# Performance work log

Measured on AMD Instinct MI355X. Metric: run time of the kernel, lower is better.

## Reference

```python
import jax, jax.numpy as jnp
import numpy as np

H, D, LORA = 12, 64, 64  # n_heads, headdim, decay-LoRA rank


def _time_mix(x, mu, w_bias, dw1, dw2, u, Wr, Wk, Wv, Wg, Wo, ln_w, ln_b):
    """RWKV-6 time-mix (single direction). x: (B,T,C)."""
    B, T, C = x.shape
    # token shift: previous token (zero-padded at t=0)
    xs = jnp.concatenate([jnp.zeros_like(x[:, :1]), x[:, :-1]], axis=1)
    dx = xs - x
    xr, xk, xv, xw, xg = (x + dx * mu[i] for i in range(5))  # order: r,k,v,w,g
    r = (xr @ Wr).reshape(B, T, H, D)
    k = (xk @ Wk).reshape(B, T, H, D)
    v = (xv @ Wv).reshape(B, T, H, D)
    g = jax.nn.silu(xg @ Wg)                                   # (B,T,C)
    # data-dependent per-channel decay in (0,1)
    w = jnp.exp(-jnp.exp(w_bias + jnp.tanh(xw @ dw1) @ dw2)).reshape(B, T, H, D)

    def step(S, rkvw):  # S: (B,H,D,D) state
        r_t, k_t, v_t, w_t = rkvw          # each (B,H,D)
        kv = k_t[..., None] * v_t[:, :, None, :]               # (B,H,D,D)
        y_t = jnp.einsum('bhd,bhde->bhe', r_t, S + u[None, :, :, None] * kv)
        return w_t[..., None] * S + kv, y_t

    seq = tuple(jnp.moveaxis(a, 1, 0) for a in (r, k, v, w))   # (T,B,H,D)
    S0 = jnp.zeros((B, H, D, D), x.dtype)
    _, ys = jax.lax.scan(step, S0, seq)
    y = jnp.moveaxis(ys, 0, 1)                                 # (B,T,H,D)
    # per-head GroupNorm (n_heads groups over d_model)
    mean = y.mean(-1, keepdims=True)
    var = y.var(-1, keepdims=True)
    y = ((y - mean) * jax.lax.rsqrt(var + 1e-5)).reshape(B, T, C) * ln_w + ln_b
    return (y * g) @ Wo


def reference(x, pad_mask, mu, w_bias, dw1, dw2, u, Wr, Wk, Wv, Wg, Wo, ln_w, ln_b):
    p = lambda i: (mu[i], w_bias[i], dw1[i], dw2[i], u[i], Wr[i], Wk[i], Wv[i],
                   Wg[i], Wo[i], ln_w[i], ln_b[i])
    fwd_out = _time_mix(x, *p(0))
    bwd_out = _time_mix(x[:, ::-1], *p(1))[:, ::-1]
    out = fwd_out + bwd_out
    out = out * pad_mask[..., None].astype(out.dtype)
    return out


def setup_inputs() -> dict:
    key = jax.random.key(0)
    ks = jax.random.split(key, 12)
    B, T, C = 4, 1024, 768
    s = C ** -0.5
    return {
        'x': jax.random.normal(ks[0], (B, T, C), jnp.float32),
        'pad_mask': jnp.ones((B, T), jnp.bool_),
        'mu': jax.random.uniform(ks[1], (2, 5, C), jnp.float32),
        'w_bias': jax.random.normal(ks[2], (2, C), jnp.float32) * 0.3 - 0.5,
        'dw1': jax.random.normal(ks[3], (2, C, LORA), jnp.float32) * s,
        'dw2': jax.random.normal(ks[4], (2, LORA, C), jnp.float32) * 0.1,
        'u': jax.random.normal(ks[5], (2, H, D), jnp.float32) * 0.5,
        'Wr': jax.random.normal(ks[6], (2, C, C), jnp.float32) * s,
        'Wk': jax.random.normal(ks[7], (2, C, C), jnp.float32) * s,
        'Wv': jax.random.normal(ks[8], (2, C, C), jnp.float32) * s,
        'Wg': jax.random.normal(ks[9], (2, C, C), jnp.float32) * s,
        'Wo': jax.random.normal(ks[10], (2, C, C), jnp.float32) * s,
        'ln_w': jnp.ones((2, C), jnp.float32),
        'ln_b': jnp.zeros((2, C), jnp.float32),
    }
```

## Files before the change

kernel.cpp:

```cpp
#include <hip/hip_runtime.h>
#include <cstdint>
#include <cstddef>


#define HH   12
#define DD   64
#define CC   768
#define TT   1024
#define BBB  4
#define LR   64
#define BT   (BBB*TT)
#define WSQ  (CC*CC)

typedef unsigned short u16;
typedef _Float16 f16x8 __attribute__((ext_vector_type(8)));
typedef float f32x4 __attribute__((ext_vector_type(4)));

__device__ __forceinline__ u16 f2h(float f) {
    const _Float16 h = (_Float16)f;
    return __builtin_bit_cast(u16, h);
}
__device__ __forceinline__ float h2f(u16 h) {
    return (float)__builtin_bit_cast(_Float16, h);
}

__device__ __forceinline__ void gl_lds16(const void* g, void* l) {
    __builtin_amdgcn_global_load_lds(
        (const __attribute__((address_space(1))) void*)g,
        (__attribute__((address_space(3))) void*)l, 16, 0, 0);
}

__device__ __forceinline__ float mask_val(const void* mp, int idx) {
    const unsigned char* b = (const unsigned char*)mp;
    const int i0 = ((const int*)mp)[0];
    if (i0 == 0x3f800000) {
        return ((const float*)mp)[idx] != 0.f ? 1.f : 0.f;
    }
    if ((b[1] | b[2] | b[3]) == 0) {
        return ((const int*)mp)[idx] != 0 ? 1.f : 0.f;
    }
    return b[idx] ? 1.f : 0.f;
}

struct TP10 { const float* src[10]; };

__global__ __launch_bounds__(256)
void transpose_conv(TP10 tj, u16* __restrict__ dst)
{
    __shared__ float sh[32][33];
    const int j = blockIdx.z;
    const float* __restrict__ src = tj.src[j];
    u16* __restrict__ d = dst + (size_t)j * WSQ;
    const int n0 = blockIdx.x << 5, k0 = blockIdx.y << 5;
    const int tx = threadIdx.x & 31, ty = threadIdx.x >> 5;
    #pragma unroll
    for (int i = 0; i < 4; ++i)
        sh[ty + (i << 3)][tx] = src[(size_t)(k0 + ty + (i << 3)) * CC + n0 + tx];
    __syncthreads();
    #pragma unroll
    for (int i = 0; i < 4; ++i)
        d[(size_t)(n0 + ty + (i << 3)) * CC + k0 + tx] =
            f2h(sh[tx][ty + (i << 3)]);
}

__global__ __launch_bounds__(256)
void convert_x(const float* __restrict__ x, u16* __restrict__ xb)
{
    const size_t off = ((size_t)blockIdx.x * 256 + threadIdx.x) * 8;
    const float4 a = *reinterpret_cast<const float4*>(x + off);
    const float4 b = *reinterpret_cast<const float4*>(x + off + 4);
    uint4 w;
    w.x = (unsigned)f2h(a.x) | ((unsigned)f2h(a.y) << 16);
    w.y = (unsigned)f2h(a.z) | ((unsigned)f2h(a.w) << 16);
    w.z = (unsigned)f2h(b.x) | ((unsigned)f2h(b.y) << 16);
    w.w = (unsigned)f2h(b.z) | ((unsigned)f2h(b.w) << 16);
    *reinterpret_cast<uint4*>(xb + off) = w;
}

__global__ __launch_bounds__(256)
void convert_mu(const float* __restrict__ mu, u16* __restrict__ muh, int n)
{
    const int i = blockIdx.x * 256 + threadIdx.x;
    if (i < n) muh[i] = f2h(mu[i]);
}

__global__ __launch_bounds__(256)
void mix4_kernel(const u16* __restrict__ xb, const u16* __restrict__ muh,
                 u16* __restrict__ mx, const int dbase)
{
    const int j = blockIdx.y;
    const int slot = blockIdx.z;
    const int dir = dbase + slot;
    const int idx = blockIdx.x * 256 + threadIdx.x;
    const int s = idx / 96;
    const int c = (idx - s * 96) << 3;
    const int b = s >> 10, ts = s & (TT - 1);
    const int t = dir ? (TT - 1 - ts) : ts;
    const int tp = dir ? (t + 1) : (t - 1);
    const int musel = (j == 3) ? 4 : j;

    const uint4 xa4 = *reinterpret_cast<const uint4*>(
        xb + (size_t)(b * TT + t) * CC + c);
    uint4 xp4 = make_uint4(0u, 0u, 0u, 0u);
    if (ts > 0)
        xp4 = *reinterpret_cast<const uint4*>(
            xb + (size_t)(b * TT + tp) * CC + c);
    const uint4 m4 = *reinterpret_cast<const uint4*>(
        muh + (size_t)dir * 5 * CC + musel * CC + c);

    const f16x8 xa = __builtin_bit_cast(f16x8, xa4);
    const f16x8 xp = __builtin_bit_cast(f16x8, xp4);
    const f16x8 mm = __builtin_bit_cast(f16x8, m4);
    const f16x8 res = (xp - xa) * mm + xa;

    u16* __restrict__ dst = mx + (size_t)((slot << 2) + j) * ((size_t)BT * CC);
    *reinterpret_cast<uint4*>(dst + (size_t)s * CC + c) =
        __builtin_bit_cast(uint4, res);
}

struct GB { const u16* Wt[8]; const u16* Ab[8]; float* out[8];
            const float* mu[8]; int act[8]; int dirv[8]; };

__global__ __launch_bounds__(256)
void gemm_mfma_big(GB p, const u16* __restrict__ xb,
                   const int K, const int N, const int mixA)
{
    const int j = blockIdx.z;
    const u16* __restrict__ Wt = p.Wt[j];
    const u16* __restrict__ Ab = p.Ab[j];
    float* __restrict__ out = p.out[j];
    const float* __restrict__ mu = p.mu[j];
    const int act = p.act[j];
    const int dir = p.dirv[j];

    __shared__ __align__(16) u16 Als[128][64];
    __shared__ __align__(16) u16 Bls[128][64];
    const int tid = threadIdx.x;
    const int rowbase = blockIdx.x << 7;
    const int colbase = blockIdx.y << 7;
    const int lane = tid & 63;
    const int wid = tid >> 6;
    const int wr = (wid >> 1) << 6;
    const int wc = (wid & 1) << 6;
    const int lm = lane & 15;

    const int lrow = lane >> 3;
    const int gcol = (((lane & 7) ^ lrow) << 3);

    f32x4 acc[4][4] = {};

    for (int k0 = 0; k0 < K; k0 += 64) {
        if (mixA) {
            #pragma unroll
            for (int it = 0; it < 4; ++it) {
                const int c   = tid + (it << 8);
                const int row = c >> 3;
                const int ch  = c & 7;
                const int kq  = (ch ^ (row & 7)) << 3;
                *reinterpret_cast<uint4*>(&Bls[row][ch << 3]) =
                    *reinterpret_cast<const uint4*>(
                        Wt + (size_t)(colbase + row) * K + k0 + kq);
                const int s  = rowbase + row;
                const int bb = s >> 10, ts = s & (TT - 1);
                const int t  = dir ? (TT - 1 - ts) : ts;
                const int tp = dir ? (t + 1) : (t - 1);
                const uint4 xa4 = *reinterpret_cast<const uint4*>(
                    xb + (size_t)(bb * TT + t) * CC + k0 + kq);
                uint4 xp4 = make_uint4(0u, 0u, 0u, 0u);
                if (ts > 0)
                    xp4 = *reinterpret_cast<const uint4*>(
                        xb + (size_t)(bb * TT + tp) * CC + k0 + kq);
                const u16* as = reinterpret_cast<const u16*>(&xa4);
                const u16* ps = reinterpret_cast<const u16*>(&xp4);
                const float4 m0 = *reinterpret_cast<const float4*>(mu + k0 + kq);
                const float4 m1 = *reinterpret_cast<const float4*>(mu + k0 + kq + 4);
                const float mm[8] = {m0.x, m0.y, m0.z, m0.w,
                                     m1.x, m1.y, m1.z, m1.w};
                uint4 w;
                unsigned rr[4];
                #pragma unroll
                for (int q = 0; q < 4; ++q) {
                    const float a0 = h2f(as[2 * q]);
                    const float a1 = h2f(as[2 * q + 1]);
                    const float p0 = h2f(ps[2 * q]);
                    const float p1 = h2f(ps[2 * q + 1]);
                    const float v0 = fmaf(p0 - a0, mm[2 * q], a0);
                    const float v1 = fmaf(p1 - a1, mm[2 * q + 1], a1);
                    rr[q] = (unsigned)f2h(v0) | ((unsigned)f2h(v1) << 16);
                }
                w.x = rr[0]; w.y = rr[1]; w.z = rr[2]; w.w = rr[3];
                *reinterpret_cast<uint4*>(&Als[row][ch << 3]) = w;
            }
        } else {
            #pragma unroll
            for (int i = 0; i < 4; ++i) {
                const int rb  = (wid << 5) + (i << 3);
                const int row = rb + lrow;
                gl_lds16(Ab + (size_t)(rowbase + row) * K + k0 + gcol,
                         &Als[rb][0]);
                gl_lds16(Wt + (size_t)(colbase + row) * K + k0 + gcol,
                         &Bls[rb][0]);
            }
        }
        __syncthreads();
        #pragma unroll
        for (int ks = 0; ks < 2; ++ks) {
            const int gc = (ks << 2) + (lane >> 4);
            const int sl = (gc ^ (lm & 7)) << 3;
            f16x8 av[4], bv[4];
            #pragma unroll
            for (int mi = 0; mi < 4; ++mi)
                av[mi] = *reinterpret_cast<const f16x8*>(
                    &Als[wr + mi * 16 + lm][sl]);
            #pragma unroll
            for (int ni = 0; ni < 4; ++ni)
                bv[ni] = *reinterpret_cast<const f16x8*>(
                    &Bls[wc + ni * 16 + lm][sl]);
            #pragma unroll
            for (int mi = 0; mi < 4; ++mi)
                #pragma unroll
                for (int ni = 0; ni < 4; ++ni)
                    acc[mi][ni] = __builtin_amdgcn_mfma_f32_16x16x32_f16(
                        av[mi], bv[ni], acc[mi][ni], 0, 0, 0);
        }
        __syncthreads();
    }

    #pragma unroll
    for (int mi = 0; mi < 4; ++mi) {
        #pragma unroll
        for (int r = 0; r < 4; ++r) {
            const int srow = rowbase + wr + mi * 16 + ((lane >> 4) << 2) + r;
            if (act <= 1) {
                #pragma unroll
                for (int ni = 0; ni < 4; ++ni) {
                    float v = acc[mi][ni][r];
                    if (act == 1) v = v / (1.f + expf(-v));
                    out[(size_t)srow * N + colbase + wc + ni * 16 + lm] = v;
                }
            } else {
                const int b2  = srow >> 10;
                const int ts2 = srow & (TT - 1);
                const int t2  = dir ? (TT - 1 - ts2) : ts2;
                float* op = out + (size_t)(b2 * TT + t2) * CC + colbase + wc + lm;
                #pragma unroll
                for (int ni = 0; ni < 4; ++ni)
                    op[ni * 16] = acc[mi][ni][r];
            }
        }
    }
}

__global__ __launch_bounds__(256)
void combine_kernel(float* __restrict__ out, const float* __restrict__ obuf,
                    const void* __restrict__ mask)
{
    const size_t idx = ((size_t)blockIdx.x * 256 + threadIdx.x) * 4;
    const int row = (int)(idx / CC);
    const float mv = mask_val(mask, row);
    const float4 a = *reinterpret_cast<const float4*>(out + idx);
    const float4 b = *reinterpret_cast<const float4*>(obuf + idx);
    *reinterpret_cast<float4*>(out + idx) = make_float4(
        (a.x + b.x) * mv, (a.y + b.y) * mv, (a.z + b.z) * mv, (a.w + b.w) * mv);
}

__global__ __launch_bounds__(256)
void lora1_kernel(const float* __restrict__ x, const float* __restrict__ mu,
                  const float* __restrict__ dw1, float* __restrict__ out,
                  const int dbase)
{
    __shared__ float As[16][68];
    __shared__ float Bs[64][68];
    const int tid = threadIdx.x;
    const int rowbase = blockIdx.x << 4;
    const int slot = blockIdx.y;
    const int dir = dbase + slot;
    const float* __restrict__ muD = mu + (size_t)dir * 5 * CC + 3 * CC;
    const float* __restrict__ dw1p = dw1 + (size_t)dir * CC * LR;
    float* __restrict__ outp = out + (size_t)slot * BT * LR;

    const int arow = tid >> 4;
    const int akq  = (tid & 15) << 2;
    const int s  = rowbase + arow;
    const int bb = s >> 10, ts = s & (TT - 1);
    const int t  = dir ? (TT - 1 - ts) : ts;
    const int tp = dir ? (t + 1) : (t - 1);

    const int c0 = tid & 63;
    const int r4 = tid >> 6;

    float acc[4] = {0.f, 0.f, 0.f, 0.f};

    for (int k0 = 0; k0 < CC; k0 += 64) {
        {
            const int c = k0 + akq;
            const float4 xa = *reinterpret_cast<const float4*>(
                x + (size_t)(bb * TT + t) * CC + c);
            float4 xp = make_float4(0.f, 0.f, 0.f, 0.f);
            if (ts > 0)
                xp = *reinterpret_cast<const float4*>(
                    x + (size_t)(bb * TT + tp) * CC + c);
            const float4 m4 = *reinterpret_cast<const float4*>(muD + c);
            float4 va;
            va.x = fmaf(xp.x - xa.x, m4.x, xa.x);
            va.y = fmaf(xp.y - xa.y, m4.y, xa.y);
            va.z = fmaf(xp.z - xa.z, m4.z, xa.z);
            va.w = fmaf(xp.w - xa.w, m4.w, xa.w);
            *reinterpret_cast<float4*>(&As[arow][akq]) = va;
        }
        #pragma unroll
        for (int it = 0; it < 4; ++it) {
            const int c2 = tid + (it << 8);
            const int brow = c2 >> 4, bcol = (c2 & 15) << 2;
            *reinterpret_cast<float4*>(&Bs[brow][bcol]) =
                *reinterpret_cast<const float4*>(
                    dw1p + (size_t)(k0 + brow) * LR + bcol);
        }
        __syncthreads();
        #pragma unroll
        for (int k4 = 0; k4 < 16; ++k4) {
            float bv[4];
            #pragma unroll
            for (int q = 0; q < 4; ++q) bv[q] = Bs[(k4 << 2) + q][c0];
            #pragma unroll
            for (int i = 0; i < 4; ++i) {
                const float4 a4 = *reinterpret_cast<const float4*>(
                    &As[r4 + (i << 2)][k4 << 2]);
                acc[i] = fmaf(a4.x, bv[0], acc[i]);
                acc[i] = fmaf(a4.y, bv[1], acc[i]);
                acc[i] = fmaf(a4.z, bv[2], acc[i]);
                acc[i] = fmaf(a4.w, bv[3], acc[i]);
            }
        }
        __syncthreads();
    }
    #pragma unroll
    for (int i = 0; i < 4; ++i)
        outp[(size_t)(rowbase + r4 + (i << 2)) * LR + c0] = tanhf(acc[i]);
}

__global__ __launch_bounds__(256)
void gemm_kernel(const float* __restrict__ lora, const float* __restrict__ dw2,
                 const float* __restrict__ wbias, float* __restrict__ wwbuf,
                 const int dbase)
{
    __shared__ float As[16][68];
    __shared__ float Bs[16][68];
    const int tid = threadIdx.x;
    const int rowbase = blockIdx.x << 6;
    const int colbase = blockIdx.y << 6;
    const int slot = blockIdx.z;
    const int dir = dbase + slot;
    const float* __restrict__ Ap = lora + (size_t)slot * BT * LR;
    const float* __restrict__ W  = dw2 + (size_t)dir * LR * CC;
    const float* __restrict__ bias = wbias + (size_t)dir * CC;
    float* __restrict__ out = wwbuf + (size_t)slot * BT * CC;

    const int ty = tid >> 4, tx = tid & 15;
    const int am = tid >> 2;
    const int aq = tid & 3;
    const int s  = rowbase + am;
    const int bk = tid >> 4;
    const int bn = (tid & 15) << 2;

    float acc[4][4];
    #pragma unroll
    for (int i = 0; i < 4; ++i)
        #pragma unroll
        for (int j = 0; j < 4; ++j) acc[i][j] = 0.f;

    for (int k0 = 0; k0 < LR; k0 += 16) {
        const float4 va = *reinterpret_cast<const float4*>(
            Ap + (size_t)s * LR + k0 + (aq << 2));
        const float4 vb = *reinterpret_cast<const float4*>(
            W + (size_t)(k0 + bk) * CC + colbase + bn);
        As[(aq << 2) + 0][am] = va.x;
        As[(aq << 2) + 1][am] = va.y;
        As[(aq << 2) + 2][am] = va.z;
        As[(aq << 2) + 3][am] = va.w;
        *reinterpret_cast<float4*>(&Bs[bk][bn]) = vb;
        __syncthreads();
        #pragma unroll
        for (int kk = 0; kk < 16; ++kk) {
            const float4 a  = *reinterpret_cast<const float4*>(&As[kk][ty << 2]);
            const float4 bv = *reinterpret_cast<const float4*>(&Bs[kk][tx << 2]);
            const float av[4]  = {a.x, a.y, a.z, a.w};
            const float bvv[4] = {bv.x, bv.y, bv.z, bv.w};
            #pragma unroll
            for (int i = 0; i < 4; ++i)
                #pragma unroll
                for (int j = 0; j < 4; ++j)
                    acc[i][j] = fmaf(av[i], bvv[j], acc[i][j]);
        }
        __syncthreads();
    }

    #pragma unroll
    for (int i = 0; i < 4; ++i) {
        const int srow = rowbase + (ty << 2) + i;
        const int ncol = colbase + (tx << 2);
        float v[4];
        #pragma unroll
        for (int j = 0; j < 4; ++j)
            v[j] = expf(-expf(acc[i][j] + bias[ncol + j]));
        *reinterpret_cast<float4*>(out + (size_t)srow * CC + ncol) =
            make_float4(v[0], v[1], v[2], v[3]);
    }
}

template<int L>
__global__ __launch_bounds__(64)
void scanA_kernel(const float* __restrict__ kbuf, const float* __restrict__ vbuf,
                  const float* __restrict__ wbuf,
                  float* __restrict__ SL, float* __restrict__ Pbuf)
{
    constexpr int NCHL = TT / L;
    constexpr size_t SLN = (size_t)NCHL * BBB * HH * DD * DD;
    constexpr size_t PN  = (size_t)NCHL * BBB * HH * DD;
    __shared__ float lk[L * DD], lw[L * DD], lv[L * DD];
    const int c = blockIdx.x, h = blockIdx.y;
    const int b = blockIdx.z & (BBB - 1);
    const int slot = blockIdx.z >> 2;
    const size_t boff = (size_t)slot * BT * CC;
    const int e = threadIdx.x;
    const int rowq = e >> 4;
    const int col  = (e & 15) << 2;

    const size_t gbase = boff + (size_t)(b * TT + c * L) * CC + h * DD;
    #pragma unroll
    for (int r4 = 0; r4 < L / 4; ++r4) {
        const int row = (r4 << 2) + rowq;
        const size_t ga = gbase + (size_t)row * CC + col;
        *reinterpret_cast<float4*>(&lk[row * DD + col]) =
            *reinterpret_cast<const float4*>(kbuf + ga);
        *reinterpret_cast<float4*>(&lw[row * DD + col]) =
            *reinterpret_cast<const float4*>(wbuf + ga);
        *reinterpret_cast<float4*>(&lv[row * DD + col]) =
            *reinterpret_cast<const float4*>(vbuf + ga);
    }
    __syncthreads();

    float S[DD];
    #pragma unroll
    for (int d = 0; d < DD; ++d) S[d] = 0.f;
    float P = 1.f;

    for (int t = 0; t < L; ++t) {
        const float ve = lv[t * DD + e];
        P *= lw[t * DD + e];
        #pragma unroll
        for (int d4 = 0; d4 < 16; ++d4) {
            const float4 k4 = *reinterpret_cast<const float4*>(&lk[t * DD + (d4 << 2)]);
            const float4 w4 = *reinterpret_cast<const float4*>(&lw[t * DD + (d4 << 2)]);
            S[(d4 << 2) + 0] = fmaf(w4.x, S[(d4 << 2) + 0], k4.x * ve);
            S[(d4 << 2) + 1] = fmaf(w4.y, S[(d4 << 2) + 1], k4.y * ve);
            S[(d4 << 2) + 2] = fmaf(w4.z, S[(d4 << 2) + 2], k4.z * ve);
            S[(d4 << 2) + 3] = fmaf(w4.w, S[(d4 << 2) + 3], k4.w * ve);
        }
    }

    float* slotp = SL + (size_t)slot * SLN
                 + (size_t)((c * BBB + b) * HH + h) * DD * DD;
    #pragma unroll
    for (int d = 0; d < DD; ++d) slotp[d * DD + e] = S[d];
    Pbuf[(size_t)slot * PN + (size_t)((c * BBB + b) * HH + h) * DD + e] = P;
}

__global__ __launch_bounds__(64)
void scanB_kernel(float* __restrict__ SL, const float* __restrict__ Pbuf,
                  const int nch)
{
    const int h = blockIdx.x, b = blockIdx.y;
    const int dg = blockIdx.z & 3;
    const int slot = blockIdx.z >> 2;
    const size_t SLN = (size_t)nch * BBB * HH * DD * DD;
    const size_t PN  = (size_t)nch * BBB * HH * DD;
    float* __restrict__ SLs = SL + (size_t)slot * SLN;
    const float* __restrict__ Ps = Pbuf + (size_t)slot * PN;
    const int e = threadIdx.x;
    const size_t doff = (size_t)dg * 16 * DD;

    float S[16];
    #pragma unroll
    for (int i = 0; i < 16; ++i) S[i] = 0.f;

    float sl[16], pp[16];
    {
        const float* s0 = SLs + (size_t)(b * HH + h) * DD * DD + doff;
        const float* p0 = Ps + (size_t)(b * HH + h) * DD + dg * 16;
        #pragma unroll
        for (int i = 0; i < 16; ++i) { sl[i] = s0[i * DD + e]; pp[i] = p0[i]; }
    }
    for (int c = 0; c < nch; ++c) {
        float sl2[16], pp2[16];
        if (c + 1 < nch) {
            const float* s1 = SLs + (size_t)(((c + 1) * BBB + b) * HH + h) * DD * DD + doff;
            const float* p1 = Ps + (size_t)(((c + 1) * BBB + b) * HH + h) * DD + dg * 16;
            #pragma unroll
            for (int i = 0; i < 16; ++i) { sl2[i] = s1[i * DD + e]; pp2[i] = p1[i]; }
        }
        float* sc = SLs + (size_t)((c * BBB + b) * HH + h) * DD * DD + doff;
        #pragma unroll
        for (int i = 0; i < 16; ++i) {
            S[i] = fmaf(pp[i], S[i], sl[i]);
            sc[i * DD + e] = S[i];
        }
        #pragma unroll
        for (int i = 0; i < 16; ++i) { sl[i] = sl2[i]; pp[i] = pp2[i]; }
    }
}

template<int L>
__global__ __launch_bounds__(64)
void scanC_kernel(const float* __restrict__ rbuf, const float* __restrict__ kbuf,
                  const float* __restrict__ vbuf, const float* __restrict__ wbuf,
                  const float* __restrict__ gbuf, const float* __restrict__ SL,
                  const float* __restrict__ u, const float* __restrict__ lnw,
                  const float* __restrict__ lnb, u16* __restrict__ zb,
                  const int dbase)
{
    constexpr int NCHL = TT / L;
    constexpr size_t SLN = (size_t)NCHL * BBB * HH * DD * DD;
    __shared__ unsigned lrk[L * DD];
    __shared__ float lw[L * DD];

    const int c = blockIdx.x, h = blockIdx.y;
    const int b = blockIdx.z & (BBB - 1);
    const int slot = blockIdx.z >> 2;
    const int dir = dbase + slot;
    const size_t boff = (size_t)slot * BT * CC;
    const int e = threadIdx.x;
    const int rowq = e >> 4;
    const int col  = (e & 15) << 2;

    const size_t gbase = boff + (size_t)(b * TT + c * L) * CC + h * DD;
    #pragma unroll
    for (int r4 = 0; r4 < L / 4; ++r4) {
        const int row = (r4 << 2) + rowq;
        const size_t ga = gbase + (size_t)row * CC + col;
        const float4 rv = *reinterpret_cast<const float4*>(rbuf + ga);
        const float4 kv = *reinterpret_cast<const float4*>(kbuf + ga);
        const float4 wv = *reinterpret_cast<const float4*>(wbuf + ga);
        *reinterpret_cast<float4*>(&lw[row * DD + col]) = wv;
        uint4 pk;
        pk.x = (unsigned)f2h(rv.x) | ((unsigned)f2h(kv.x) << 16);
        pk.y = (unsigned)f2h(rv.y) | ((unsigned)f2h(kv.y) << 16);
        pk.z = (unsigned)f2h(rv.z) | ((unsigned)f2h(kv.z) << 16);
        pk.w = (unsigned)f2h(rv.w) | ((unsigned)f2h(kv.w) << 16);
        *reinterpret_cast<uint4*>(&lrk[row * DD + col]) = pk;
    }
    __syncthreads();

    const float ue = u[(size_t)(dir * HH + h) * DD + e];
    const float gw = lnw[dir * CC + h * DD + e];
    const float gb = lnb[dir * CC + h * DD + e];

    float S[DD];
    if (c == 0) {
        #pragma unroll
        for (int d = 0; d < DD; ++d) S[d] = 0.f;
    } else {
        const float* slotp = SL + (size_t)slot * SLN
                           + (size_t)(((c - 1) * BBB + b) * HH + h) * DD * DD;
        #pragma unroll
        for (int d = 0; d < DD; ++d) S[d] = slotp[d * DD + e];
    }

    float ve = vbuf[gbase + e];
    float ge = gbuf[gbase + e];
    for (int t = 0; t < L; ++t) {
        float ve2 = 0.f, ge2 = 0.f;
        if (t + 1 < L) {
            ve2 = vbuf[gbase + (size_t)(t + 1) * CC + e];
            ge2 = gbuf[gbase + (size_t)(t + 1) * CC + e];
        }
        const unsigned rke = lrk[t * DD + e];
        float coef = h2f((u16)(rke & 0xffffu)) * ue * h2f((u16)(rke >> 16));
        #pragma unroll
        for (int off = 32; off > 0; off >>= 1) coef += __shfl_xor(coef, off);

        float y0 = 0.f, y1 = 0.f, y2 = 0.f, y3 = 0.f;
        #pragma unroll
        for (int d4 = 0; d4 < 16; ++d4) {
            const uint4 rk4 = *reinterpret_cast<const uint4*>(
                &lrk[t * DD + (d4 << 2)]);
            const float4 w4 = *reinterpret_cast<const float4*>(
                &lw[t * DD + (d4 << 2)]);
            const float r0 = h2f((u16)(rk4.x & 0xffffu)), k0 = h2f((u16)(rk4.x >> 16));
            const float r1 = h2f((u16)(rk4.y & 0xffffu)), k1 = h2f((u16)(rk4.y >> 16));
            const float r2 = h2f((u16)(rk4.z & 0xffffu)), k2 = h2f((u16)(rk4.z >> 16));
            const float r3 = h2f((u16)(rk4.w & 0xffffu)), k3 = h2f((u16)(rk4.w >> 16));
            y0 = fmaf(r0, S[(d4 << 2) + 0], y0);
            y1 = fmaf(r1, S[(d4 << 2) + 1], y1);
            y2 = fmaf(r2, S[(d4 << 2) + 2], y2);
            y3 = fmaf(r3, S[(d4 << 2) + 3], y3);
            S[(d4 << 2) + 0] = fmaf(w4.x, S[(d4 << 2) + 0], k0 * ve);
            S[(d4 << 2) + 1] = fmaf(w4.y, S[(d4 << 2) + 1], k1 * ve);
            S[(d4 << 2) + 2] = fmaf(w4.z, S[(d4 << 2) + 2], k2 * ve);
            S[(d4 << 2) + 3] = fmaf(w4.w, S[(d4 << 2) + 3], k3 * ve);
        }
        float y = ((y0 + y1) + (y2 + y3)) + coef * ve;

        float sum = y, sq = y * y;
        #pragma unroll
        for (int off = 32; off > 0; off >>= 1) {
            sum += __shfl_xor(sum, off);
            sq  += __shfl_xor(sq, off);
        }
        const float mean = sum * (1.f / 64.f);
        const float var  = fmaf(-mean, mean, sq * (1.f / 64.f));
        const float yn   = (y - mean) * rsqrtf(var + 1e-5f) * gw + gb;
        zb[gbase + (size_t)t * CC + e] = f2h(yn * ge);
        ve = ve2;
        ge = ge2;
    }
}

extern "C" void kernel_launch(void* const* d_in, const int* in_sizes, int n_in,
                              void* d_out, int out_size, void* d_ws, size_t ws_size,
                              hipStream_t stream)
{
    const float* x     = (const float*)d_in[0];
    const void*  mask  = d_in[1];
    const float* mu    = (const float*)d_in[2];
    const float* wbias = (const float*)d_in[3];
    const float* dw1   = (const float*)d_in[4];
    const float* dw2   = (const float*)d_in[5];
    const float* u     = (const float*)d_in[6];
    const float* Wr    = (const float*)d_in[7];
    const float* Wk    = (const float*)d_in[8];
    const float* Wv    = (const float*)d_in[9];
    const float* Wg    = (const float*)d_in[10];
    const float* Wo    = (const float*)d_in[11];
    const float* lnw   = (const float*)d_in[12];
    const float* lnb   = (const float*)d_in[13];
    float* out = (float*)d_out;

    float* ws = (float*)d_ws;
    const size_t NBT = (size_t)BT * CC;
    const size_t MUN = 2 * 5 * CC;

    auto plan = [&](int nd, int nch, bool mb, bool& alias) -> size_t {
        const size_t SLN = (size_t)nch * BBB * HH * DD * DD;
        const size_t PN  = (size_t)nch * BBB * HH * DD;
        const size_t slp = (size_t)nd * (SLN + PN) * 4;
        const size_t mxb = mb ? (size_t)4 * nd * NBT * 2 : 0;
        alias = mb && slp >= mxb;
        return ((size_t)5 * nd * NBT + (size_t)nd * BT * LR) * 4
             + slp
             + ((size_t)nd * NBT + NBT + (size_t)10 * WSQ + MUN) * 2
             + (alias ? 0 : mxb);
    };
    int nd = 1, nch = 16; bool mixbuf = false, alias = false;
    {
        bool a;
        if      (plan(2, 64, true, a) <= ws_size) { nd = 2; nch = 64; mixbuf = true; alias = a; }
        else if (plan(2, 32, true, a) <= ws_size) { nd = 2; nch = 32; mixbuf = true; alias = a; }
        else if (plan(2, 16, true, a) <= ws_size) { nd = 2; nch = 16; mixbuf = true; alias = a; }
        else {
            nd = 1;
            mixbuf = plan(1, 16, true, a) <= ws_size;
            if (mixbuf) alias = a;
            nch = (plan(1, 64, mixbuf, a) <= ws_size) ? 64
                : (plan(1, 32, mixbuf, a) <= ws_size) ? 32 : 16;
            bool a2; (void)plan(1, nch, mixbuf, a2); alias = mixbuf && a2;
        }
    }
    const size_t SLN = (size_t)nch * BBB * HH * DD * DD;
    const size_t PN  = (size_t)nch * BBB * HH * DD;

    float* rbuf  = ws;
    float* kbuf  = rbuf  + (size_t)nd * NBT;
    float* vbuf  = kbuf  + (size_t)nd * NBT;
    float* wwbuf = vbuf  + (size_t)nd * NBT;
    float* gbuf  = wwbuf + (size_t)nd * NBT;
    float* lora  = gbuf  + (size_t)nd * NBT;
    float* SL    = lora  + (size_t)nd * BT * LR;
    float* Pbuf  = SL    + (size_t)nd * SLN;
    u16*   zb    = (u16*)(Pbuf + (size_t)nd * PN);
    u16*   xbb   = zb + (size_t)nd * NBT;
    u16*   wtb   = xbb + NBT;
    u16*   muh   = wtb + (size_t)10 * WSQ;
    u16*   mx    = alias ? (u16*)SL : (muh + MUN);
    float* obuf  = rbuf;

    TP10 tj;
    const float* Wlist[5] = {Wr, Wk, Wv, Wg, Wo};
    for (int dir = 0; dir < 2; ++dir)
        for (int i = 0; i < 5; ++i)
            tj.src[dir * 5 + i] = Wlist[i] + (size_t)dir * WSQ;
    transpose_conv<<<dim3(24, 24, 10), 256, 0, stream>>>(tj, wtb);
    convert_x<<<dim3((int)(NBT / (8 * 256))), 256, 0, stream>>>(x, xbb);
    convert_mu<<<dim3((int)((MUN + 255) / 256)), 256, 0, stream>>>(mu, muh, (int)MUN);

    auto launch_scans = [&](int ndl, int dbase) {
        if (nch == 64) {
            scanA_kernel<16><<<dim3(64, HH, BBB * ndl), dim3(64), 0, stream>>>(
                kbuf, vbuf, wwbuf, SL, Pbuf);
            scanB_kernel<<<dim3(HH, BBB, 4 * ndl), dim3(64), 0, stream>>>(SL, Pbuf, 64);
            scanC_kernel<16><<<dim3(64, HH, BBB * ndl), dim3(64), 0, stream>>>(
                rbuf, kbuf, vbuf, wwbuf, gbuf, SL, u, lnw, lnb, zb, dbase);
        } else if (nch == 32) {
            scanA_kernel<32><<<dim3(32, HH, BBB * ndl), dim3(64), 0, stream>>>(
                kbuf, vbuf, wwbuf, SL, Pbuf);
            scanB_kernel<<<dim3(HH, BBB, 4 * ndl), dim3(64), 0, stream>>>(SL, Pbuf, 32);
            scanC_kernel<32><<<dim3(32, HH, BBB * ndl), dim3(64), 0, stream>>>(
                rbuf, kbuf, vbuf, wwbuf, gbuf, SL, u, lnw, lnb, zb, dbase);
        } else {
            scanA_kernel<64><<<dim3(16, HH, BBB * ndl), dim3(64), 0, stream>>>(
                kbuf, vbuf, wwbuf, SL, Pbuf);
            scanB_kernel<<<dim3(HH, BBB, 4 * ndl), dim3(64), 0, stream>>>(SL, Pbuf, 16);
            scanC_kernel<64><<<dim3(16, HH, BBB * ndl), dim3(64), 0, stream>>>(
                rbuf, kbuf, vbuf, wwbuf, gbuf, SL, u, lnw, lnb, zb, dbase);
        }
    };

    if (nd == 2) {
        mix4_kernel<<<dim3((int)(NBT / (8 * 256)), 4, 2), 256, 0, stream>>>(
            xbb, muh, mx, 0);

        GB pb;
        float* outs[4] = {rbuf, kbuf, vbuf, gbuf};
        for (int s = 0; s < 2; ++s) {
            const u16* wt = wtb + (size_t)s * 5 * WSQ;
            for (int j = 0; j < 4; ++j) {
                const int jj = s * 4 + j;
                pb.Wt[jj]  = wt + (size_t)j * WSQ;
                pb.Ab[jj]  = mx + (size_t)jj * NBT;
                pb.out[jj] = outs[j] + (size_t)s * NBT;
                pb.mu[jj]  = mu;
                pb.act[jj] = (j == 3) ? 1 : 0;
                pb.dirv[jj] = s;
            }
        }
        gemm_mfma_big<<<dim3(BT / 128, CC / 128, 8), 256, 0, stream>>>(
            pb, xbb, CC, CC, 0);

        lora1_kernel<<<dim3(BT / 16, 2), 256, 0, stream>>>(x, mu, dw1, lora, 0);
        gemm_kernel<<<dim3(BT / 64, CC / 64, 2), 256, 0, stream>>>(
            lora, dw2, wbias, wwbuf, 0);

        launch_scans(2, 0);

        GB po = {};
        for (int s = 0; s < 2; ++s) {
            po.Wt[s]  = wtb + (size_t)s * 5 * WSQ + (size_t)4 * WSQ;
            po.Ab[s]  = zb + (size_t)s * NBT;
            po.out[s] = (s == 0) ? out : obuf;
            po.mu[s]  = mu;
            po.act[s] = 4;
            po.dirv[s] = s;
        }
        gemm_mfma_big<<<dim3(BT / 128, CC / 128, 2), 256, 0, stream>>>(
            po, xbb, CC, CC, 0);
    } else {
        for (int d = 0; d < 2; ++d) {
            const u16* wt = wtb + (size_t)d * 5 * WSQ;
            GB pb;
            float* outs[4] = {rbuf, kbuf, vbuf, gbuf};
            for (int j = 0; j < 4; ++j) {
                pb.Wt[j]  = wt + (size_t)j * WSQ;
                pb.Ab[j]  = mx + (size_t)j * NBT;
                pb.out[j] = outs[j];
                pb.mu[j]  = mu + (size_t)d * 5 * CC + (size_t)((j == 3) ? 4 : j) * CC;
                pb.act[j] = (j == 3) ? 1 : 0;
                pb.dirv[j] = d;
            }
            if (mixbuf) {
                mix4_kernel<<<dim3((int)(NBT / (8 * 256)), 4, 1), 256, 0, stream>>>(
                    xbb, muh, mx, d);
                gemm_mfma_big<<<dim3(BT / 128, CC / 128, 4), 256, 0, stream>>>(
                    pb, xbb, CC, CC, 0);
            } else {
                gemm_mfma_big<<<dim3(BT / 128, CC / 128, 4), 256, 0, stream>>>(
                    pb, xbb, CC, CC, 1);
            }
            lora1_kernel<<<dim3(BT / 16, 1), 256, 0, stream>>>(x, mu, dw1, lora, d);
            gemm_kernel<<<dim3(BT / 64, CC / 64, 1), 256, 0, stream>>>(
                lora, dw2, wbias, wwbuf, d);

            launch_scans(1, d);

            GB po = {};
            po.Wt[0]  = wt + (size_t)4 * WSQ;
            po.Ab[0]  = zb;
            po.out[0] = (d == 0) ? out : obuf;
            po.mu[0]  = mu;
            po.act[0] = 4;
            po.dirv[0] = d;
            gemm_mfma_big<<<dim3(BT / 128, CC / 128, 1), 256, 0, stream>>>(
                po, xbb, CC, CC, 0);
        }
    }

    combine_kernel<<<dim3((int)(NBT / (4 * 256))), 256, 0, stream>>>(
        out, obuf, mask);
}
```

Baseline: 345.8 us.

## Split scanC state rows across two waves and drop 64-chunk scan option

The chunked-scan output kernel now runs 128 threads per block. Each wave holds half of the 64 state rows, so per-thread state registers drop from 64 to 32, and the partial outputs are combined through shared memory with a block barrier every timestep. Wave 0 alone does the bonus term, the GroupNorm and the store. The nch=64 configuration (16-token chunks) is removed, so the default becomes 32 chunks of 32 tokens. This trades more parallelism and lower register pressure for a per-step __syncthreads and an idle second wave during normalization.

Measured after the change: 328.6 us. -5.0%, faster.

```diff
diff --git a/kernel.cpp b/kernel.cpp
--- a/kernel.cpp
+++ b/kernel.cpp
@@ -511,7 +511,7 @@
 }
 
 template<int L>
-__global__ __launch_bounds__(64)
+__global__ __launch_bounds__(128)
 void scanC_kernel(const float* __restrict__ rbuf, const float* __restrict__ kbuf,
                   const float* __restrict__ vbuf, const float* __restrict__ wbuf,
                   const float* __restrict__ gbuf, const float* __restrict__ SL,
@@ -523,31 +523,37 @@
     constexpr size_t SLN = (size_t)NCHL * BBB * HH * DD * DD;
     __shared__ unsigned lrk[L * DD];
     __shared__ float lw[L * DD];
+    __shared__ float pys[2][DD];
 
     const int c = blockIdx.x, h = blockIdx.y;
     const int b = blockIdx.z & (BBB - 1);
     const int slot = blockIdx.z >> 2;
     const int dir = dbase + slot;
     const size_t boff = (size_t)slot * BT * CC;
-    const int e = threadIdx.x;
-    const int rowq = e >> 4;
-    const int col  = (e & 15) << 2;
+    const int tid = threadIdx.x;
+    const int e = tid & 63;
+    const int w = tid >> 6;
+    const int db = w << 5;
 
     const size_t gbase = boff + (size_t)(b * TT + c * L) * CC + h * DD;
-    #pragma unroll
-    for (int r4 = 0; r4 < L / 4; ++r4) {
-        const int row = (r4 << 2) + rowq;
-        const size_t ga = gbase + (size_t)row * CC + col;
-        const float4 rv = *reinterpret_cast<const float4*>(rbuf + ga);
-        const float4 kv = *reinterpret_cast<const float4*>(kbuf + ga);
-        const float4 wv = *reinterpret_cast<const float4*>(wbuf + ga);
-        *reinterpret_cast<float4*>(&lw[row * DD + col]) = wv;
-        uint4 pk;
-        pk.x = (unsigned)f2h(rv.x) | ((unsigned)f2h(kv.x) << 16);
-        pk.y = (unsigned)f2h(rv.y) | ((unsigned)f2h(kv.y) << 16);
-        pk.z = (unsigned)f2h(rv.z) | ((unsigned)f2h(kv.z) << 16);
-        pk.w = (unsigned)f2h(rv.w) | ((unsigned)f2h(kv.w) << 16);
-        *reinterpret_cast<uint4*>(&lrk[row * DD + col]) = pk;
+    {
+        const int rowq = tid >> 4;
+        const int col  = (tid & 15) << 2;
+        #pragma unroll
+        for (int r8 = 0; r8 < L / 8; ++r8) {
+            const int row = (r8 << 3) + rowq;
+            const size_t ga = gbase + (size_t)row * CC + col;
+            const float4 rv = *reinterpret_cast<const float4*>(rbuf + ga);
+            const float4 kv = *reinterpret_cast<const float4*>(kbuf + ga);
+            const float4 wv = *reinterpret_cast<const float4*>(wbuf + ga);
+            *reinterpret_cast<float4*>(&lw[row * DD + col]) = wv;
+            uint4 pk;
+            pk.x = (unsigned)f2h(rv.x) | ((unsigned)f2h(kv.x) << 16);
+            pk.y = (unsigned)f2h(rv.y) | ((unsigned)f2h(kv.y) << 16);
+            pk.z = (unsigned)f2h(rv.z) | ((unsigned)f2h(kv.z) << 16);
+            pk.w = (unsigned)f2h(rv.w) | ((unsigned)f2h(kv.w) << 16);
+            *reinterpret_cast<uint4*>(&lrk[row * DD + col]) = pk;
+        }
     }
     __syncthreads();
 
@@ -555,62 +561,65 @@
     const float gw = lnw[dir * CC + h * DD + e];
     const float gb = lnb[dir * CC + h * DD + e];
 
-    float S[DD];
+    float S[32];
     if (c == 0) {
         #pragma unroll
-        for (int d = 0; d < DD; ++d) S[d] = 0.f;
+        for (int i = 0; i < 32; ++i) S[i] = 0.f;
     } else {
         const float* slotp = SL + (size_t)slot * SLN
                            + (size_t)(((c - 1) * BBB + b) * HH + h) * DD * DD;
         #pragma unroll
-        for (int d = 0; d < DD; ++d) S[d] = slotp[d * DD + e];
+        for (int i = 0; i < 32; ++i) S[i] = slotp[(db + i) * DD + e];
     }
 
     float ve = vbuf[gbase + e];
-    float ge = gbuf[gbase + e];
+    float ge = (w == 0) ? gbuf[gbase + e] : 0.f;
     for (int t = 0; t < L; ++t) {
         float ve2 = 0.f, ge2 = 0.f;
         if (t + 1 < L) {
             ve2 = vbuf[gbase + (size_t)(t + 1) * CC + e];
-            ge2 = gbuf[gbase + (size_t)(t + 1) * CC + e];
-        }
-        const unsigned rke = lrk[t * DD + e];
-        float coef = h2f((u16)(rke & 0xffffu)) * ue * h2f((u16)(rke >> 16));
-        #pragma unroll
-        for (int off = 32; off > 0; off >>= 1) coef += __shfl_xor(coef, off);
-
+            if (w == 0) ge2 = gbuf[gbase + (size_t)(t + 1) * CC + e];
+        }
         float y0 = 0.f, y1 = 0.f, y2 = 0.f, y3 = 0.f;
         #pragma unroll
-        for (int d4 = 0; d4 < 16; ++d4) {
-            const uint4 rk4 = *reinterpret_cast<const uint4*>(
-                &lrk[t * DD + (d4 << 2)]);
-            const float4 w4 = *reinterpret_cast<const float4*>(
-                &lw[t * DD + (d4 << 2)]);
+        for (int d8 = 0; d8 < 8; ++d8) {
+            const int dd = db + (d8 << 2);
+            const uint4 rk4 = *reinterpret_cast<const uint4*>(&lrk[t * DD + dd]);
+            const float4 w4 = *reinterpret_cast<const float4*>(&lw[t * DD + dd]);
             const float r0 = h2f((u16)(rk4.x & 0xffffu)), k0 = h2f((u16)(rk4.x >> 16));
             const float r1 = h2f((u16)(rk4.y & 0xffffu)), k1 = h2f((u16)(rk4.y >> 16));
             const float r2 = h2f((u16)(rk4.z & 0xffffu)), k2 = h2f((u16)(rk4.z >> 16));
             const float r3 = h2f((u16)(rk4.w & 0xffffu)), k3 = h2f((u16)(rk4.w >> 16));
-            y0 = fmaf(r0, S[(d4 << 2) + 0], y0);
-            y1 = fmaf(r1, S[(d4 << 2) + 1], y1);
-            y2 = fmaf(r2, S[(d4 << 2) + 2], y2);
-            y3 = fmaf(r3, S[(d4 << 2) + 3], y3);
-            S[(d4 << 2) + 0] = fmaf(w4.x, S[(d4 << 2) + 0], k0 * ve);
-            S[(d4 << 2) + 1] = fmaf(w4.y, S[(d4 << 2) + 1], k1 * ve);
-            S[(d4 << 2) + 2] = fmaf(w4.z, S[(d4 << 2) + 2], k2 * ve);
-            S[(d4 << 2) + 3] = fmaf(w4.w, S[(d4 << 2) + 3], k3 * ve);
-        }
-        float y = ((y0 + y1) + (y2 + y3)) + coef * ve;
-
-        float sum = y, sq = y * y;
-        #pragma unroll
-        for (int off = 32; off > 0; off >>= 1) {
-            sum += __shfl_xor(sum, off);
-            sq  += __shfl_xor(sq, off);
-        }
-        const float mean = sum * (1.f / 64.f);
-        const float var  = fmaf(-mean, mean, sq * (1.f / 64.f));
-        const float yn   = (y - mean) * rsqrtf(var + 1e-5f) * gw + gb;
-        zb[gbase + (size_t)t * CC + e] = f2h(yn * ge);
+            y0 = fmaf(r0, S[(d8 << 2) + 0], y0);
+            y1 = fmaf(r1, S[(d8 << 2) + 1], y1);
+            y2 = fmaf(r2, S[(d8 << 2) + 2], y2);
+            y3 = fmaf(r3, S[(d8 << 2) + 3], y3);
+            S[(d8 << 2) + 0] = fmaf(w4.x, S[(d8 << 2) + 0], k0 * ve);
+            S[(d8 << 2) + 1] = fmaf(w4.y, S[(d8 << 2) + 1], k1 * ve);
+            S[(d8 << 2) + 2] = fmaf(w4.z, S[(d8 << 2) + 2], k2 * ve);
+            S[(d8 << 2) + 3] = fmaf(w4.w, S[(d8 << 2) + 3], k3 * ve);
+        }
+        const float yp = (y0 + y1) + (y2 + y3);
+        if (w == 1) pys[t & 1][e] = yp;
+        __syncthreads();
+        if (w == 0) {
+            const unsigned rke = lrk[t * DD + e];
+            float coef = h2f((u16)(rke & 0xffffu)) * ue * h2f((u16)(rke >> 16));
+            #pragma unroll
+            for (int off = 32; off > 0; off >>= 1) coef += __shfl_xor(coef, off);
+
+            float y = yp + pys[t & 1][e] + coef * ve;
+            float sum = y, sq = y * y;
+            #pragma unroll
+            for (int off = 32; off > 0; off >>= 1) {
+                sum += __shfl_xor(sum, off);
+                sq  += __shfl_xor(sq, off);
+            }
+            const float mean = sum * (1.f / 64.f);
+            const float var  = fmaf(-mean, mean, sq * (1.f / 64.f));
+            const float yn   = (y - mean) * rsqrtf(var + 1e-5f) * gw + gb;
+            zb[gbase + (size_t)t * CC + e] = f2h(yn * ge);
+        }
         ve = ve2;
         ge = ge2;
     }
@@ -654,15 +663,13 @@
     int nd = 1, nch = 16; bool mixbuf = false, alias = false;
     {
         bool a;
-        if      (plan(2, 64, true, a) <= ws_size) { nd = 2; nch = 64; mixbuf = true; alias = a; }
-        else if (plan(2, 32, true, a) <= ws_size) { nd = 2; nch = 32; mixbuf = true; alias = a; }
+        if      (plan(2, 32, true, a) <= ws_size) { nd = 2; nch = 32; mixbuf = true; alias = a; }
         else if (plan(2, 16, true, a) <= ws_size) { nd = 2; nch = 16; mixbuf = true; alias = a; }
         else {
             nd = 1;
             mixbuf = plan(1, 16, true, a) <= ws_size;
             if (mixbuf) alias = a;
-            nch = (plan(1, 64, mixbuf, a) <= ws_size) ? 64
-                : (plan(1, 32, mixbuf, a) <= ws_size) ? 32 : 16;
+            nch = (plan(1, 32, mixbuf, a) <= ws_size) ? 32 : 16;
             bool a2; (void)plan(1, nch, mixbuf, a2); alias = mixbuf && a2;
         }
     }
@@ -694,23 +701,17 @@
     convert_mu<<<dim3((int)((MUN + 255) / 256)), 256, 0, stream>>>(mu, muh, (int)MUN);
 
     auto launch_scans = [&](int ndl, int dbase) {
-        if (nch == 64) {
-            scanA_kernel<16><<<dim3(64, HH, BBB * ndl), dim3(64), 0, stream>>>(
-                kbuf, vbuf, wwbuf, SL, Pbuf);
-            scanB_kernel<<<dim3(HH, BBB, 4 * ndl), dim3(64), 0, stream>>>(SL, Pbuf, 64);
-            scanC_kernel<16><<<dim3(64, HH, BBB * ndl), dim3(64), 0, stream>>>(
-                rbuf, kbuf, vbuf, wwbuf, gbuf, SL, u, lnw, lnb, zb, dbase);
-        } else if (nch == 32) {
+        if (nch == 32) {
             scanA_kernel<32><<<dim3(32, HH, BBB * ndl), dim3(64), 0, stream>>>(
                 kbuf, vbuf, wwbuf, SL, Pbuf);
             scanB_kernel<<<dim3(HH, BBB, 4 * ndl), dim3(64), 0, stream>>>(SL, Pbuf, 32);
-            scanC_kernel<32><<<dim3(32, HH, BBB * ndl), dim3(64), 0, stream>>>(
+            scanC_kernel<32><<<dim3(32, HH, BBB * ndl), dim3(128), 0, stream>>>(
                 rbuf, kbuf, vbuf, wwbuf, gbuf, SL, u, lnw, lnb, zb, dbase);
         } else {
             scanA_kernel<64><<<dim3(16, HH, BBB * ndl), dim3(64), 0, stream>>>(
                 kbuf, vbuf, wwbuf, SL, Pbuf);
             scanB_kernel<<<dim3(HH, BBB, 4 * ndl), dim3(64), 0, stream>>>(SL, Pbuf, 16);
-            scanC_kernel<64><<<dim3(16, HH, BBB * ndl), dim3(64), 0, stream>>>(
+            scanC_kernel<64><<<dim3(16, HH, BBB * ndl), dim3(128), 0, stream>>>(
                 rbuf, kbuf, vbuf, wwbuf, gbuf, SL, u, lnw, lnb, zb, dbase);
         }
     };
```
